# Kernel optimization log

Measured on AMD Instinct MI355X. Metric: run time of the kernel, lower is better.

The kernel has to match this reference:

```python
import jax, jax.numpy as jnp
import numpy as np

N_NODES = 100000
N_EDGES = 1600000
N_GRAPHS = 512
N_REL = 4
N_TYPES = 13
EMB = 128
HID = 128
BN_EPS = 1e-5
L2_EPS = 1e-12


def setup_inputs() -> dict:
    key = jax.random.key(0)
    ks = jax.random.split(key, 16)
    node_type = jax.random.randint(ks[0], (N_NODES,), 0, N_TYPES)
    x = jax.nn.one_hot(node_type, N_TYPES, dtype=jnp.float32)  # [N,13] one-hot
    edge_index = jax.random.randint(ks[1], (2, N_EDGES), 0, N_NODES)
    edge_type = jax.random.randint(ks[2], (N_EDGES,), 0, N_REL)
    batch = jnp.sort(jax.random.randint(ks[3], (N_NODES,), 0, N_GRAPHS))
    s = 0.05
    return {
        "x": x,
        "edge_index": edge_index,
        "edge_type": edge_type,
        "batch": batch,
        "emb": jax.random.normal(ks[4], (N_TYPES, EMB), jnp.float32) * s,
        "Wrel": jax.random.normal(ks[5], (2, N_REL, HID, HID), jnp.float32) * s,  # layer0 in=EMB==HID
        "Wroot": jax.random.normal(ks[6], (2, HID, HID), jnp.float32) * s,
        "conv_bias": jnp.zeros((2, HID), jnp.float32),
        "bn_gamma": jnp.ones((2, HID), jnp.float32),
        "bn_beta": jnp.zeros((2, HID), jnp.float32),
        "prelu_a": jnp.full((2,), 0.25, jnp.float32),
        "fc1_w": jax.random.normal(ks[7], (HID, 256), jnp.float32) * s,
        "fc1_b": jnp.zeros((256,), jnp.float32),
        "fc2_w": jax.random.normal(ks[8], (256, 128), jnp.float32) * s,
        "fc2_b": jnp.zeros((128,), jnp.float32),
        "out_w": jax.random.normal(ks[9], (128, 1), jnp.float32) * s,
        "out_b": jnp.zeros((1,), jnp.float32),
    }


def _rgcn_conv(h, Wrel, Wroot, bias, src, dst, edge_type):
    # PyG RGCNConv: out = h @ Wroot + bias + sum_r mean_{edges of rel r}(h_src @ W_r)
    n = h.shape[0]
    out = h @ Wroot + bias
    for r in range(N_REL):
        m = (edge_type == r).astype(h.dtype)  # [E]
        hr = h @ Wrel[r]                       # [N, dout]
        msg = hr[src] * m[:, None]             # gather + mask  [E, dout]
        num = jax.ops.segment_sum(msg, dst, num_segments=n)
        cnt = jax.ops.segment_sum(m, dst, num_segments=n)
        out = out + num / jnp.maximum(cnt, 1.0)[:, None]
    return out


def _batchnorm(h, gamma, beta):
    mu = jnp.mean(h, axis=0)
    var = jnp.mean((h - mu) ** 2, axis=0)  # biased var (training-mode BN)
    return (h - mu) * jax.lax.rsqrt(var + BN_EPS) * gamma + beta


def reference(x, edge_index, edge_type, batch, emb, Wrel, Wroot, conv_bias,
              bn_gamma, bn_beta, prelu_a, fc1_w, fc1_b, fc2_w, fc2_b, out_w, out_b):
    src, dst = edge_index[0], edge_index[1]
    idx = jnp.argmax(x, axis=1)         # torch.nonzero(one_hot)[1]
    h = emb[idx]                        # [N, EMB]
    for l in range(2):
        h = _rgcn_conv(h, Wrel[l], Wroot[l], conv_bias[l], src, dst, edge_type)
        h = _batchnorm(h, bn_gamma[l], bn_beta[l])
        h = jnp.where(h >= 0, h, prelu_a[l] * h)  # PReLU
        nrm = jnp.sqrt(jnp.sum(h * h, axis=1, keepdims=True))
        h = h / jnp.maximum(nrm, L2_EPS)          # F.normalize(p=2, dim=1)
    # global mean pool over graphs
    pooled = jax.ops.segment_sum(h, batch, num_segments=N_GRAPHS)
    cnt = jax.ops.segment_sum(jnp.ones((h.shape[0],), h.dtype), batch, num_segments=N_GRAPHS)
    g = pooled / jnp.maximum(cnt, 1.0)[:, None]   # [G, HID]
    g = jax.nn.relu(g @ fc1_w + fc1_b)
    g = jax.nn.relu(g @ fc2_w + fc2_b)
    return g @ out_w + out_b                      # [G, 1]
```

## Files before the change

### kernel.cpp

```cpp
#include <hip/hip_runtime.h>
#include <hip/hip_bf16.h>

#define NN 100000
#define NE 1600000
#define NG 512
#define CH3 65536
#define CHW 16384
#define NCH 2
#define BPC 128
#define ES 12500


typedef __attribute__((ext_vector_type(8))) short short8;
typedef __attribute__((ext_vector_type(4))) float float4v;


__device__ inline int lower_bound_dev(const int* __restrict__ a, int n, int v) {
    int lo = 0, hi = n;
    while (lo < hi) { int mid = (lo + hi) >> 1; if (a[mid] < v) lo = mid + 1; else hi = mid; }
    return lo;
}

__device__ inline unsigned short f2bf(float x) {
    unsigned u = __float_as_uint(x);
    unsigned r = (u + 0x7fffu + ((u >> 16) & 1u)) >> 16;
    return (unsigned short)r;
}


__global__ void node_type_kernel(const float* __restrict__ x, int* __restrict__ idx, int n) {
    int i = blockIdx.x * blockDim.x + threadIdx.x;
    if (i >= n) return;
    const float* row = x + (size_t)i * 13;
    int b = 0;
    #pragma unroll
    for (int t = 0; t < 13; ++t) if (row[t] > 0.5f) { b = t; }
    idx[i] = b;
}


__global__ void build_weights(const float* __restrict__ emb, const float* __restrict__ Wroot,
                              const float* __restrict__ Wrel,
                              unsigned short* __restrict__ Bf, unsigned short* __restrict__ B0f,
                              float* __restrict__ bnSums, float* __restrict__ bnSums1,
                              float* __restrict__ g0) {
    if (blockIdx.x < 8) bnSums[blockIdx.x * 256 + threadIdx.x] = 0.f;
    else if (blockIdx.x < 16) bnSums1[(blockIdx.x - 8) * 256 + threadIdx.x] = 0.f;
    int i = blockIdx.x * 256 + threadIdx.x;
    if (i < 81920) {
        int j = i & 7;
        int lane = (i >> 3) & 63;
        int t = (i >> 9) & 7;
        int ks = (i >> 12) & 3;
        int kc = i >> 14;
        int n = t * 16 + (lane & 15);
        int kcol = j * 16 + ks * 4 + (lane >> 4);
        float w;
        if (kc == 0) w = Wroot[16384 + (size_t)kcol * 128 + n];
        else {
            int r = kc - 1;
            w = Wrel[(((size_t)(4 + r) * 128) + kcol) * 128 + n];
        }
        Bf[i] = f2bf(w);
    } else if (i < 94208) {
        int i0 = i - 81920;
        int j = i0 & 7;
        int lane = (i0 >> 3) & 63;
        int t = (i0 >> 9) & 7;
        int ks = i0 >> 12;
        int n = t * 16 + (lane & 15);
        int p = ks * 32 + (lane >> 4) * 8 + j;
        float val = 0.f;
        if (p < 32) {
            if (p < 13) {
                const float* er = emb + (size_t)p * 128;
                const float* wc = Wroot + n;
                float acc = 0.f;
                for (int k = 0; k < 128; ++k) acc += er[k] * wc[(size_t)k * 128];
                val = acc;
            }
        } else {
            int r = (p - 32) >> 4, tt = (p - 32) & 15;
            if (tt < 13) {
                const float* er = emb + (size_t)tt * 128;
                const float* wc = Wrel + ((size_t)r * 128) * 128 + n;
                float acc = 0.f;
                for (int k = 0; k < 128; ++k) acc += er[k] * wc[(size_t)k * 128];
                val = acc;
            }
        }
        B0f[i0] = f2bf(val);
    } else {
        int gz = i - 94208;
        g0[gz] = 0.f;
    }
}


__global__ __launch_bounds__(256) void hist_kernel(const int* __restrict__ dst,
                                                   const int* __restrict__ src,
                                                   const int* __restrict__ et,
                                                   const int* __restrict__ ntype,
                                                   int* __restrict__ srcT,
                                                   unsigned* __restrict__ partials) {
    __shared__ unsigned h[CHW];
    const int b = blockIdx.x, c = blockIdx.y;
    const int lo = c * CH3;
    for (int i = threadIdx.x; i < CHW; i += 256) h[i] = 0;
    __syncthreads();
    const int e0 = b * ES;
    const int e1 = (e0 + ES < NE) ? e0 + ES : NE;
    if (c == 0) {
        for (int e = e0 + threadIdx.x; e < e1; e += 256) {
            int k = dst[e] - lo;
            if (k >= 0 && k < CH3) atomicAdd(&h[k >> 2], 1u << ((k & 3) << 3));
            int s = src[e];
            srcT[e] = s | (ntype[s] << 17) | (et[e] << 21);
        }
    } else {
        for (int e = e0 + threadIdx.x; e < e1; e += 256) {
            int k = dst[e] - lo;
            if (k >= 0 && k < CH3) atomicAdd(&h[k >> 2], 1u << ((k & 3) << 3));
        }
    }
    __syncthreads();
    unsigned* out = partials + ((size_t)(c * BPC + b)) * CHW;
    for (int i = threadIdx.x; i < CHW; i += 256) out[i] = h[i];
}

__global__ void hist_reduce(unsigned* __restrict__ partials, int* __restrict__ counts) {
    const int c = blockIdx.y;
    const int i = blockIdx.x * 256 + threadIdx.x;
    size_t base = (size_t)c * BPC * CHW + i;
    unsigned r0 = 0, r1 = 0, r2 = 0, r3 = 0;
    #pragma unroll 4
    for (int b = 0; b < BPC; ++b) {
        unsigned t = partials[base + (size_t)b * CHW];
        partials[base + (size_t)b * CHW] = r0 | (r1 << 8) | (r2 << 16) | (r3 << 24);
        r0 += t & 0xffu; r1 += (t >> 8) & 0xffu; r2 += (t >> 16) & 0xffu; r3 += t >> 24;
    }
    int k0 = c * CH3 + 4 * i;
    if (k0 < NN)     counts[k0]     = (int)r0;
    if (k0 + 1 < NN) counts[k0 + 1] = (int)r1;
    if (k0 + 2 < NN) counts[k0 + 2] = (int)r2;
    if (k0 + 3 < NN) counts[k0 + 3] = (int)r3;
}

__global__ __launch_bounds__(256) void scan1(const int* __restrict__ counts, int* __restrict__ offs,
                                             int* __restrict__ bsums, int n) {
    __shared__ int wsum[4];
    const int base = blockIdx.x * 1024 + threadIdx.x * 4;
    int v[4]; int loc = 0;
    #pragma unroll
    for (int j = 0; j < 4; ++j) { int idx = base + j; v[j] = (idx < n) ? counts[idx] : 0; loc += v[j]; }
    const int lane = threadIdx.x & 63, wid = threadIdx.x >> 6;
    int sc = loc;
    #pragma unroll
    for (int o = 1; o < 64; o <<= 1) { int t = __shfl_up(sc, o, 64); if (lane >= o) sc += t; }
    if (lane == 63) wsum[wid] = sc;
    __syncthreads();
    int wbase = 0;
    for (int w = 0; w < wid; ++w) wbase += wsum[w];
    int run = wbase + sc - loc;
    #pragma unroll
    for (int j = 0; j < 4; ++j) { int idx = base + j; if (idx < n) offs[idx] = run; run += v[j]; }
    if (threadIdx.x == 255) bsums[blockIdx.x] = wbase + sc;
}

__global__ void scan2(int* __restrict__ bsums, int* __restrict__ offs, int nb, int n) {
    const int lane = threadIdx.x;
    int carry = 0;
    for (int base = 0; base < nb; base += 64) {
        int idx = base + lane;
        int v = (idx < nb) ? bsums[idx] : 0;
        int sc = v;
        #pragma unroll
        for (int o = 1; o < 64; o <<= 1) { int t = __shfl_up(sc, o, 64); if (lane >= o) sc += t; }
        if (idx < nb) bsums[idx] = carry + sc - v;
        int tot = __shfl(sc, 63, 64);
        carry += tot;
    }
    if (lane == 0) offs[n] = carry;
}

__global__ __launch_bounds__(256) void scan3(int* __restrict__ offs, const int* __restrict__ bsums, int n) {
    const int s = bsums[blockIdx.x];
    const int base = blockIdx.x * 1024 + threadIdx.x * 4;
    #pragma unroll
    for (int j = 0; j < 4; ++j) { int idx = base + j; if (idx < n) offs[idx] += s; }
}

__global__ __launch_bounds__(256) void place_kernel(const int* __restrict__ dst,
                                                    const int* __restrict__ srcT,
                                                    const int* __restrict__ offs,
                                                    const unsigned* __restrict__ partials,
                                                    int* __restrict__ sortedSrc) {
    __shared__ unsigned cur[CHW];
    const int b = blockIdx.x, c = blockIdx.y;
    const int lo = c * CH3;
    const unsigned* pb = partials + ((size_t)(c * BPC + b)) * CHW;
    for (int i = threadIdx.x; i < CHW; i += 256) cur[i] = pb[i];
    __syncthreads();
    const int e0 = b * ES;
    const int e1 = (e0 + ES < NE) ? e0 + ES : NE;
    for (int e = e0 + threadIdx.x; e < e1; e += 256) {
        int key = dst[e];
        int k = key - lo;
        if (k >= 0 && k < CH3) {
            int sh = (k & 3) << 3;
            unsigned old = atomicAdd(&cur[k >> 2], 1u << sh);
            int my = (int)((old >> sh) & 0xffu);
            int pos = offs[key] + my;
            sortedSrc[pos] = srcT[e];
        }
    }
}


__global__ __launch_bounds__(256) void gemm0_fused(const int* __restrict__ sortedSrc,
                                                   const int* __restrict__ offs,
                                                   const int* __restrict__ ntype,
                                                   const unsigned short* __restrict__ B0f,
                                                   const float* __restrict__ bias,
                                                   unsigned short* __restrict__ Cb,
                                                   float* __restrict__ bnSums, int M) {
    __shared__ unsigned short A0L[12 * 128 * 8];
    __shared__ unsigned cnt[128][13];
    __shared__ float sred[2][4][128];
    const int tid = threadIdx.x;

    if (tid < 128) {
        const int n = blockIdx.x * 128 + tid;
        const int tile = tid >> 4, l16 = tid & 15;
        if (n < M) {
            #pragma unroll
            for (int t = 0; t < 13; ++t) cnt[tid][t] = 0;
            const int o0 = offs[n], o1 = offs[n + 1];
            unsigned relc = 0;
            for (int i = o0; i < o1; ++i) {
                int v = sortedSrc[i];
                int ty = (v >> 17) & 15, r = v >> 21;
                cnt[tid][ty] += 1u << (r << 3);
                relc += 1u << (r << 3);
            }
            float inv[4];
            #pragma unroll
            for (int r = 0; r < 4; ++r) {
                unsigned c = (relc >> (r << 3)) & 0xffu;
                inv[r] = 1.0f / (float)(c > 0 ? c : 1);
            }
            const int myty = ntype[n];
            #pragma unroll
            for (int ks = 0; ks < 3; ++ks) {
                #pragma unroll
                for (int quad = 0; quad < 4; ++quad) {
                    unsigned short vals[8];
                    #pragma unroll
                    for (int j = 0; j < 8; ++j) {
                        int p = ks * 32 + quad * 8 + j;
                        float v;
                        if (p < 32) v = (p == myty) ? 1.0f : 0.0f;
                        else {
                            int r = (p - 32) >> 4, tt = (p - 32) & 15;
                            v = (tt < 13) ? (float)((cnt[tid][tt] >> (r << 3)) & 0xffu) * inv[r] : 0.0f;
                        }
                        vals[j] = f2bf(v);
                    }
                    const int C = ks * 4 + quad;
                    *(uint4*)(A0L + (C * 128 + tile * 16 + l16) * 8) = *(uint4*)vals;
                }
            }
        } else {
            uint4 z; z.x = 0; z.y = 0; z.z = 0; z.w = 0;
            #pragma unroll
            for (int C = 0; C < 12; ++C)
                *(uint4*)(A0L + (C * 128 + tile * 16 + l16) * 8) = z;
        }
    }
    __syncthreads();

    const int wv = tid >> 6, lane = tid & 63;
    const int l16 = lane & 15, quad = lane >> 4;
    const int rowbase = blockIdx.x * 128 + wv * 32;
    const int tileL0 = wv * 2, tileL1 = wv * 2 + 1;

    float4v acc[2][8];
    #pragma unroll
    for (int t = 0; t < 8; ++t) {
        float bv = bias[t * 16 + l16];
        float4v av = {bv, bv, bv, bv};
        acc[0][t] = av; acc[1][t] = av;
    }

    const unsigned short* bl = B0f + lane * 8;
    #pragma unroll
    for (int ks = 0; ks < 3; ++ks) {
        const int C = ks * 4 + quad;
        short8 af0 = *(const short8*)(A0L + (C * 128 + tileL0 * 16 + l16) * 8);
        short8 af1 = *(const short8*)(A0L + (C * 128 + tileL1 * 16 + l16) * 8);
        const unsigned short* bp = bl + ((ks * 8) << 9);
        #pragma unroll
        for (int t = 0; t < 8; ++t) {
            short8 bf = *(const short8*)(bp + (t << 9));
            acc[0][t] = __builtin_amdgcn_mfma_f32_16x16x32_bf16(af0, bf, acc[0][t], 0, 0, 0);
            acc[1][t] = __builtin_amdgcn_mfma_f32_16x16x32_bf16(af1, bf, acc[1][t], 0, 0, 0);
        }
    }

    #pragma unroll
    for (int h = 0; h < 2; ++h) {
        #pragma unroll
        for (int rg = 0; rg < 4; ++rg) {
            int rr = rowbase + h * 16 + quad * 4 + rg;
            if (rr < M) {
                unsigned short v[8];
                #pragma unroll
                for (int t = 0; t < 8; ++t) v[t] = f2bf(acc[h][t][rg]);
                *(uint4*)(Cb + (size_t)rr * 128 + l16 * 8) = *(uint4*)v;
            }
        }
    }
    float s[8], q[8];
    #pragma unroll
    for (int t = 0; t < 8; ++t) {
        s[t] = 0.f; q[t] = 0.f;
        #pragma unroll
        for (int h = 0; h < 2; ++h) {
            #pragma unroll
            for (int rg = 0; rg < 4; ++rg) {
                int rr = rowbase + h * 16 + quad * 4 + rg;
                if (rr < M) { float v = acc[h][t][rg]; s[t] += v; q[t] += v * v; }
            }
        }
    }
    #pragma unroll
    for (int t = 0; t < 8; ++t) {
        s[t] += __shfl_down(s[t], 32, 64); q[t] += __shfl_down(q[t], 32, 64);
        s[t] += __shfl_down(s[t], 16, 64); q[t] += __shfl_down(q[t], 16, 64);
    }
    if (lane < 16) {
        #pragma unroll
        for (int t = 0; t < 8; ++t) {
            sred[0][wv][t * 16 + l16] = s[t];
            sred[1][wv][t * 16 + l16] = q[t];
        }
    }
    __syncthreads();
    if (tid < 128) {
        float S = sred[0][0][tid] + sred[0][1][tid] + sred[0][2][tid] + sred[0][3][tid];
        float Q = sred[1][0][tid] + sred[1][1][tid] + sred[1][2][tid] + sred[1][3][tid];
        float* bnS = bnSums + ((blockIdx.x & 7) << 8);
        unsafeAtomicAdd(bnS + tid, S);
        unsafeAtomicAdd(bnS + 128 + tid, Q);
    }
}


__global__ __launch_bounds__(256) void gather_gemm1(const unsigned short* __restrict__ hbf,
                                                    const int* __restrict__ sortedSrc,
                                                    const int* __restrict__ offs,
                                                    const unsigned short* __restrict__ Bf,
                                                    const float* __restrict__ bias,
                                                    unsigned short* __restrict__ Cb,
                                                    float* __restrict__ bnSums) {
    __shared__ unsigned short rootL[2048];
    __shared__ unsigned short aggL[8192];
    const int tid = threadIdx.x;
    const int tile = blockIdx.x;
    {
        const int l16g = tid >> 4;
        const int cidx = tid & 15;
        const int c8 = cidx << 3;
        const int n = tile * 16 + l16g;
        const int pu = cidx * 16 + (l16g ^ cidx);
        uint4 ru = *(const uint4*)(hbf + (size_t)n * 128 + c8);
        *(uint4*)(rootL + pu * 8) = ru;

        const unsigned short* hb = hbf + c8;
        const int o0 = offs[n], o1 = offs[n + 1];

        float a0[8], a1[8], a2[8], a3[8];
        #pragma unroll
        for (int j = 0; j < 8; ++j) { a0[j] = 0.f; a1[j] = 0.f; a2[j] = 0.f; a3[j] = 0.f; }
        float c0 = 0.f, c1 = 0.f, c2 = 0.f, c3 = 0.f;

        auto body = [&](int v, uint4 u) {
            int r = v >> 21;
            float f[8];
            f[0] = __uint_as_float(u.x << 16); f[1] = __uint_as_float(u.x & 0xffff0000u);
            f[2] = __uint_as_float(u.y << 16); f[3] = __uint_as_float(u.y & 0xffff0000u);
            f[4] = __uint_as_float(u.z << 16); f[5] = __uint_as_float(u.z & 0xffff0000u);
            f[6] = __uint_as_float(u.w << 16); f[7] = __uint_as_float(u.w & 0xffff0000u);
            float m0 = (r == 0) ? 1.f : 0.f, m1 = (r == 1) ? 1.f : 0.f;
            float m2 = (r == 2) ? 1.f : 0.f, m3 = (r == 3) ? 1.f : 0.f;
            c0 += m0; c1 += m1; c2 += m2; c3 += m3;
            #pragma unroll
            for (int j = 0; j < 8; ++j) {
                a0[j] = fmaf(m0, f[j], a0[j]);
                a1[j] = fmaf(m1, f[j], a1[j]);
                a2[j] = fmaf(m2, f[j], a2[j]);
                a3[j] = fmaf(m3, f[j], a3[j]);
            }
        };

        int i = o0;
        for (; i + 4 <= o1; i += 4) {
            int v0 = sortedSrc[i], v1 = sortedSrc[i + 1];
            int v2 = sortedSrc[i + 2], v3 = sortedSrc[i + 3];
            uint4 u0 = *(const uint4*)(hb + (size_t)(v0 & 0x1ffff) * 128);
            uint4 u1 = *(const uint4*)(hb + (size_t)(v1 & 0x1ffff) * 128);
            uint4 u2 = *(const uint4*)(hb + (size_t)(v2 & 0x1ffff) * 128);
            uint4 u3 = *(const uint4*)(hb + (size_t)(v3 & 0x1ffff) * 128);
            body(v0, u0); body(v1, u1); body(v2, u2); body(v3, u3);
        }
        if (i + 2 <= o1) {
            int v0 = sortedSrc[i], v1 = sortedSrc[i + 1];
            uint4 u0 = *(const uint4*)(hb + (size_t)(v0 & 0x1ffff) * 128);
            uint4 u1 = *(const uint4*)(hb + (size_t)(v1 & 0x1ffff) * 128);
            body(v0, u0); body(v1, u1);
            i += 2;
        }
        if (i < o1) {
            int v0 = sortedSrc[i];
            uint4 u0 = *(const uint4*)(hb + (size_t)(v0 & 0x1ffff) * 128);
            body(v0, u0);
        }

        const float i0 = 1.f / fmaxf(c0, 1.f), i1 = 1.f / fmaxf(c1, 1.f);
        const float i2 = 1.f / fmaxf(c2, 1.f), i3 = 1.f / fmaxf(c3, 1.f);
        unsigned short* bp = aggL + pu * 8;
        auto pack = [&](float* a, float inv, unsigned short* dp) {
            unsigned short v[8];
            #pragma unroll
            for (int j = 0; j < 8; ++j) v[j] = f2bf(a[j] * inv);
            *(uint4*)dp = *(uint4*)v;
        };
        pack(a0, i0, bp);
        pack(a1, i1, bp + 2048);
        pack(a2, i2, bp + 4096);
        pack(a3, i3, bp + 6144);
    }
    __syncthreads();

    const int wv = tid >> 6, lane = tid & 63;
    const int l16 = lane & 15, quad = lane >> 4;
    const int t0 = wv << 1;
    float4v acc0, acc1;
    {
        float b0v = bias[t0 * 16 + l16];
        float b1v = bias[(t0 + 1) * 16 + l16];
        float4v a0v = {b0v, b0v, b0v, b0v};
        float4v a1v = {b1v, b1v, b1v, b1v};
        acc0 = a0v; acc1 = a1v;
    }
    const unsigned short* bl = Bf + lane * 8;
    #pragma unroll
    for (int kc = 0; kc < 5; ++kc) {
        const unsigned short* Abase = (kc == 0) ? rootL : (aggL + (kc - 1) * 2048);
        #pragma unroll
        for (int ks = 0; ks < 4; ++ks) {
            const int C = ks * 4 + quad;
            const int p = C * 16 + (l16 ^ C);
            short8 af = *(const short8*)(Abase + p * 8);
            const unsigned short* bp = bl + (((kc * 4 + ks) * 8 + t0) << 9);
            short8 b0 = *(const short8*)(bp);
            short8 b1 = *(const short8*)(bp + 512);
            acc0 = __builtin_amdgcn_mfma_f32_16x16x32_bf16(af, b0, acc0, 0, 0, 0);
            acc1 = __builtin_amdgcn_mfma_f32_16x16x32_bf16(af, b1, acc1, 0, 0, 0);
        }
    }
    const int rowbase = tile * 16;
    #pragma unroll
    for (int rg = 0; rg < 4; ++rg) {
        int rr = rowbase + quad * 4 + rg;
        unsigned pk = (unsigned)f2bf(acc0[rg]) | ((unsigned)f2bf(acc1[rg]) << 16);
        *(unsigned*)(Cb + (size_t)rr * 128 + l16 * 8 + t0) = pk;
    }
    float s0 = 0.f, q0 = 0.f, s1 = 0.f, q1 = 0.f;
    #pragma unroll
    for (int rg = 0; rg < 4; ++rg) {
        float v0 = acc0[rg], v1 = acc1[rg];
        s0 += v0; q0 += v0 * v0; s1 += v1; q1 += v1 * v1;
    }
    s0 += __shfl_down(s0, 32, 64); q0 += __shfl_down(q0, 32, 64);
    s1 += __shfl_down(s1, 32, 64); q1 += __shfl_down(q1, 32, 64);
    s0 += __shfl_down(s0, 16, 64); q0 += __shfl_down(q0, 16, 64);
    s1 += __shfl_down(s1, 16, 64); q1 += __shfl_down(q1, 16, 64);
    if (lane < 16) {
        float* bnS = bnSums + ((tile & 7) << 8);
        unsafeAtomicAdd(bnS + t0 * 16 + l16, s0);
        unsafeAtomicAdd(bnS + 128 + t0 * 16 + l16, q0);
        unsafeAtomicAdd(bnS + (t0 + 1) * 16 + l16, s1);
        unsafeAtomicAdd(bnS + 128 + (t0 + 1) * 16 + l16, q1);
    }
}


__global__ __launch_bounds__(256) void bn_apply_kernel(const unsigned short* __restrict__ Cb,
                                unsigned short* __restrict__ hbf,
                                const float* __restrict__ bnSums,
                                const float* __restrict__ gamma, const float* __restrict__ beta,
                                const float* __restrict__ prelu_a, int layer) {
    __shared__ float finS[256];
    const int tid = threadIdx.x;
    if (tid < 128) {
        float s = 0.f, q = 0.f;
        #pragma unroll
        for (int j = 0; j < 8; ++j) { s += bnSums[j * 256 + tid]; q += bnSums[j * 256 + 128 + tid]; }
        const float invn = 1.0f / (float)NN;
        float mu = s * invn;
        float var = q * invn - mu * mu; if (var < 0.f) var = 0.f;
        finS[tid] = mu;
        finS[128 + tid] = rsqrtf(var + 1e-5f);
    }
    __syncthreads();
    const int row = blockIdx.x * 16 + (tid >> 4);
    const int li = tid & 15;
    const int p8 = li << 3;
    const float a = prelu_a[layer];
    uint4 u = *(const uint4*)(Cb + (size_t)row * 128 + p8);
    float v[8];
    v[0] = __uint_as_float(u.x << 16); v[1] = __uint_as_float(u.x & 0xffff0000u);
    v[2] = __uint_as_float(u.y << 16); v[3] = __uint_as_float(u.y & 0xffff0000u);
    v[4] = __uint_as_float(u.z << 16); v[5] = __uint_as_float(u.z & 0xffff0000u);
    v[6] = __uint_as_float(u.w << 16); v[7] = __uint_as_float(u.w & 0xffff0000u);
    float t[8]; float ss = 0.f;
    #pragma unroll
    for (int j = 0; j < 8; ++j) {
        int cc = j * 16 + li;
        float tv = (v[j] - finS[cc]) * finS[128 + cc] * gamma[cc] + beta[cc];
        tv = (tv >= 0.f) ? tv : a * tv;
        t[j] = tv; ss += tv * tv;
    }
    ss += __shfl_xor(ss, 1, 64);
    ss += __shfl_xor(ss, 2, 64);
    ss += __shfl_xor(ss, 4, 64);
    ss += __shfl_xor(ss, 8, 64);
    const float scale = 1.0f / fmaxf(sqrtf(ss), 1e-12f);
    unsigned short o[8];
    #pragma unroll
    for (int j = 0; j < 8; ++j) o[j] = f2bf(t[j] * scale);
    *(uint4*)(hbf + (size_t)row * 128 + p8) = *(uint4*)o;
}


__global__ __launch_bounds__(256) void bn_apply_pool(const unsigned short* __restrict__ Cb,
                                const float* __restrict__ bnSums,
                                const float* __restrict__ gamma, const float* __restrict__ beta,
                                const float* __restrict__ prelu_a,
                                const int* __restrict__ batch,
                                float* __restrict__ g0) {
    __shared__ float P[16][128];
    __shared__ int gids[16];
    __shared__ float finS[256];
    const int tid = threadIdx.x;
    if (tid < 128) {
        float s = 0.f, q = 0.f;
        #pragma unroll
        for (int j = 0; j < 8; ++j) { s += bnSums[j * 256 + tid]; q += bnSums[j * 256 + 128 + tid]; }
        const float invn = 1.0f / (float)NN;
        float mu = s * invn;
        float var = q * invn - mu * mu; if (var < 0.f) var = 0.f;
        finS[tid] = mu;
        finS[128 + tid] = rsqrtf(var + 1e-5f);
    }
    const int r16 = tid >> 4;
    const int li = tid & 15;
    const int row = blockIdx.x * 16 + r16;
    const int p8 = li << 3;
    if (li == 0) gids[r16] = batch[row];
    __syncthreads();
    const float a = prelu_a[1];
    uint4 u = *(const uint4*)(Cb + (size_t)row * 128 + p8);
    float v[8];
    v[0] = __uint_as_float(u.x << 16); v[1] = __uint_as_float(u.x & 0xffff0000u);
    v[2] = __uint_as_float(u.y << 16); v[3] = __uint_as_float(u.y & 0xffff0000u);
    v[4] = __uint_as_float(u.z << 16); v[5] = __uint_as_float(u.z & 0xffff0000u);
    v[6] = __uint_as_float(u.w << 16); v[7] = __uint_as_float(u.w & 0xffff0000u);
    float t[8]; float ss = 0.f;
    #pragma unroll
    for (int j = 0; j < 8; ++j) {
        int cc = j * 16 + li;
        float tv = (v[j] - finS[cc]) * finS[128 + cc] * gamma[cc] + beta[cc];
        tv = (tv >= 0.f) ? tv : a * tv;
        t[j] = tv; ss += tv * tv;
    }
    ss += __shfl_xor(ss, 1, 64);
    ss += __shfl_xor(ss, 2, 64);
    ss += __shfl_xor(ss, 4, 64);
    ss += __shfl_xor(ss, 8, 64);
    const float scale = 1.0f / fmaxf(sqrtf(ss), 1e-12f);
    #pragma unroll
    for (int j = 0; j < 8; ++j) P[r16][p8 + j] = t[j] * scale;
    __syncthreads();
    if (tid < 128) {
        int cur = gids[0];
        float run = 0.f;
        #pragma unroll
        for (int rr = 0; rr < 16; ++rr) {
            int g = gids[rr];
            if (g != cur) {
                unsafeAtomicAdd(&g0[(size_t)cur * 128 + tid], run);
                run = 0.f; cur = g;
            }
            run += P[rr][tid];
        }
        unsafeAtomicAdd(&g0[(size_t)cur * 128 + tid], run);
    }
}


__global__ void fc1_kernel(const float* __restrict__ g, const float* __restrict__ w,
                           const float* __restrict__ b, const int* __restrict__ batch,
                           float* __restrict__ o) {
    __shared__ int se[2];
    const int row = blockIdx.x;
    const int j = threadIdx.x;
    if (j < 2) se[j] = lower_bound_dev(batch, NN, row + j);
    __syncthreads();
    const int c = se[1] - se[0];
    const float invc = 1.0f / (float)(c > 0 ? c : 1);
    float acc = 0.f;
    #pragma unroll 8
    for (int k = 0; k < 128; ++k) {
        int lk = (k & 7) * 16 + (k >> 3);
        acc += g[row * 128 + k] * w[lk * 256 + j];
    }
    o[row * 256 + j] = fmaxf(acc * invc + b[j], 0.f);
}

__global__ void fc2_kernel(const float* __restrict__ g, const float* __restrict__ w,
                           const float* __restrict__ b, float* __restrict__ o) {
    const int row = blockIdx.x;
    const int j = threadIdx.x;
    float acc = b[j];
    #pragma unroll 8
    for (int k = 0; k < 256; ++k) acc += g[row * 256 + k] * w[k * 128 + j];
    o[row * 128 + j] = fmaxf(acc, 0.f);
}

__global__ void fco_kernel(const float* __restrict__ g, const float* __restrict__ w,
                           const float* __restrict__ b, float* __restrict__ o) {
    const int row = blockIdx.x * blockDim.x + threadIdx.x;
    if (row >= NG) return;
    float acc = b[0];
    #pragma unroll 8
    for (int k = 0; k < 128; ++k) acc += g[row * 128 + k] * w[k];
    o[row] = acc;
}


extern "C" void kernel_launch(void* const* d_in, const int* in_sizes, int n_in,
                              void* d_out, int out_size, void* d_ws, size_t ws_size,
                              hipStream_t stream) {
    const float* x      = (const float*)d_in[0];
    const int*   eidx   = (const int*)d_in[1];
    const int*   etype  = (const int*)d_in[2];
    const int*   batch  = (const int*)d_in[3];
    const float* emb    = (const float*)d_in[4];
    const float* Wrel   = (const float*)d_in[5];
    const float* Wroot  = (const float*)d_in[6];
    const float* cbias  = (const float*)d_in[7];
    const float* gamma  = (const float*)d_in[8];
    const float* beta   = (const float*)d_in[9];
    const float* prelua = (const float*)d_in[10];
    const float* fc1w   = (const float*)d_in[11];
    const float* fc1b   = (const float*)d_in[12];
    const float* fc2w   = (const float*)d_in[13];
    const float* fc2b   = (const float*)d_in[14];
    const float* outw   = (const float*)d_in[15];
    const float* outb   = (const float*)d_in[16];
    float* out = (float*)d_out;

    const int* src = eidx;
    const int* dst = eidx + NE;

    char* p = (char*)d_ws;
    auto alloc = [&](size_t bytes) { char* r = p; p += (bytes + 255) & ~(size_t)255; return r; };
    unsigned short* hbf   = (unsigned short*)alloc((size_t)NN * 128 * 2);
    unsigned short* Cb    = (unsigned short*)alloc((size_t)NN * 128 * 2);
    unsigned* partials = (unsigned*)alloc((size_t)NCH * BPC * CHW * 4);
    int*   sortedSrc = (int*)alloc((size_t)NE * 4);
    int*   srcT      = (int*)alloc((size_t)NE * 4);
    int*   offs      = (int*)alloc((size_t)(NN + 1) * 4);
    int*   bsums     = (int*)alloc(1024);
    int*   ntype     = (int*)alloc((size_t)NN * 4);
    unsigned short* Bf1 = (unsigned short*)alloc((size_t)81920 * 2);
    unsigned short* B0f = (unsigned short*)alloc((size_t)12288 * 2);
    float* bnSums  = (float*)alloc(2048 * 4);
    float* bnSums1 = (float*)alloc(2048 * 4);
    float* g0      = (float*)alloc((size_t)NG * 128 * 4);
    float* g1      = (float*)alloc((size_t)NG * 256 * 4);
    float* g2      = (float*)alloc((size_t)NG * 128 * 4);

    const int NBLK = (NN + 1023) / 1024;

    node_type_kernel<<<(NN + 255) / 256, 256, 0, stream>>>(x, ntype, NN);
    build_weights<<<624, 256, 0, stream>>>(emb, Wroot, Wrel, Bf1, B0f, bnSums, bnSums1, g0);

    hist_kernel<<<dim3(BPC, NCH), 256, 0, stream>>>(dst, src, etype, ntype, srcT, partials);
    hist_reduce<<<dim3(CHW / 256, NCH), 256, 0, stream>>>(partials, offs);
    scan1<<<NBLK, 256, 0, stream>>>(offs, offs, bsums, NN);
    scan2<<<1, 64, 0, stream>>>(bsums, offs, NBLK, NN);
    scan3<<<NBLK, 256, 0, stream>>>(offs, bsums, NN);
    place_kernel<<<dim3(BPC, NCH), 256, 0, stream>>>(dst, srcT, offs, partials, sortedSrc);

    gemm0_fused<<<(NN + 127) / 128, 256, 0, stream>>>(sortedSrc, offs, ntype, B0f,
                                                      cbias, Cb, bnSums, NN);
    bn_apply_kernel<<<NN / 16, 256, 0, stream>>>(Cb, hbf, bnSums, gamma, beta, prelua, 0);

    gather_gemm1<<<NN / 16, 256, 0, stream>>>(hbf, sortedSrc, offs, Bf1, cbias + 128, Cb, bnSums1);
    bn_apply_pool<<<NN / 16, 256, 0, stream>>>(Cb, bnSums1, gamma + 128, beta + 128,
                                               prelua, batch, g0);

    fc1_kernel<<<NG, 256, 0, stream>>>(g0, fc1w, fc1b, batch, g1);
    fc2_kernel<<<NG, 128, 0, stream>>>(g1, fc2w, fc2b, g2);
    fco_kernel<<<2, 256, 0, stream>>>(g2, outw, outb, out);
}
```

Baseline: 359.3 us.

## Precompute per-node type/relation counts in histogram pass; fuse scans and fc2/out

Layer 0 needs, for each destination node, counts of incoming edges per source node type and relation. These counts are now accumulated with global atomics inside the histogram kernel (zeroed in node_type_kernel), so gemm0 reads a compact count table instead of walking the sorted CSR. The change also merges the two-stage scan carry propagation into one kernel where each block sums the preceding block totals, and fuses fc2 with the final output projection. This removes a serial per-node loop over edges and two kernel launches, in exchange for 1.6M extra global atomics and a 5MB count buffer.

Result: slower. 400.2 us (+11.4%).

```diff
diff --git a/kernel.cpp b/kernel.cpp
--- a/kernel.cpp
+++ b/kernel.cpp
@@ -28,7 +28,8 @@
 }
 
 
-__global__ void node_type_kernel(const float* __restrict__ x, int* __restrict__ idx, int n) {
+__global__ void node_type_kernel(const float* __restrict__ x, int* __restrict__ idx,
+                                 unsigned* __restrict__ cntG, int n) {
     int i = blockIdx.x * blockDim.x + threadIdx.x;
     if (i >= n) return;
     const float* row = x + (size_t)i * 13;
@@ -36,6 +37,9 @@
     #pragma unroll
     for (int t = 0; t < 13; ++t) if (row[t] > 0.5f) { b = t; }
     idx[i] = b;
+    unsigned* c = cntG + (size_t)i * 13;
+    #pragma unroll
+    for (int t = 0; t < 13; ++t) c[t] = 0u;
 }
 
 
@@ -102,6 +106,7 @@
                                                    const int* __restrict__ et,
                                                    const int* __restrict__ ntype,
                                                    int* __restrict__ srcT,
+                                                   unsigned* __restrict__ cntG,
                                                    unsigned* __restrict__ partials) {
     __shared__ unsigned h[CHW];
     const int b = blockIdx.x, c = blockIdx.y;
@@ -112,10 +117,14 @@
     const int e1 = (e0 + ES < NE) ? e0 + ES : NE;
     if (c == 0) {
         for (int e = e0 + threadIdx.x; e < e1; e += 256) {
-            int k = dst[e] - lo;
+            int d = dst[e];
+            int k = d - lo;
             if (k >= 0 && k < CH3) atomicAdd(&h[k >> 2], 1u << ((k & 3) << 3));
             int s = src[e];
-            srcT[e] = s | (ntype[s] << 17) | (et[e] << 21);
+            int ty = ntype[s];
+            int r = et[e];
+            srcT[e] = s | (ty << 17) | (r << 21);
+            atomicAdd(&cntG[(size_t)d * 13 + ty], 1u << (r << 3));
         }
     } else {
         for (int e = e0 + threadIdx.x; e < e1; e += 256) {
@@ -167,27 +176,23 @@
     if (threadIdx.x == 255) bsums[blockIdx.x] = wbase + sc;
 }
 
-__global__ void scan2(int* __restrict__ bsums, int* __restrict__ offs, int nb, int n) {
-    const int lane = threadIdx.x;
-    int carry = 0;
-    for (int base = 0; base < nb; base += 64) {
-        int idx = base + lane;
-        int v = (idx < nb) ? bsums[idx] : 0;
-        int sc = v;
-        #pragma unroll
-        for (int o = 1; o < 64; o <<= 1) { int t = __shfl_up(sc, o, 64); if (lane >= o) sc += t; }
-        if (idx < nb) bsums[idx] = carry + sc - v;
-        int tot = __shfl(sc, 63, 64);
-        carry += tot;
-    }
-    if (lane == 0) offs[n] = carry;
-}
-
-__global__ __launch_bounds__(256) void scan3(int* __restrict__ offs, const int* __restrict__ bsums, int n) {
-    const int s = bsums[blockIdx.x];
-    const int base = blockIdx.x * 1024 + threadIdx.x * 4;
+__global__ __launch_bounds__(256) void scan23(int* __restrict__ offs, const int* __restrict__ bsums,
+                                              int nb, int n) {
+    __shared__ int part[256];
+    const int tid = threadIdx.x;
+    int v = (tid < nb && tid < blockIdx.x) ? bsums[tid] : 0;
+    part[tid] = v;
+    __syncthreads();
+    #pragma unroll
+    for (int o = 128; o > 0; o >>= 1) {
+        if (tid < o) part[tid] += part[tid + o];
+        __syncthreads();
+    }
+    const int s = part[0];
+    const int base = blockIdx.x * 1024 + tid * 4;
     #pragma unroll
     for (int j = 0; j < 4; ++j) { int idx = base + j; if (idx < n) offs[idx] += s; }
+    if (blockIdx.x == (unsigned)(nb - 1) && tid == 0) offs[n] = s + bsums[nb - 1];
 }
 
 __global__ __launch_bounds__(256) void place_kernel(const int* __restrict__ dst,
@@ -217,32 +222,30 @@
 }
 
 
-__global__ __launch_bounds__(256) void gemm0_fused(const int* __restrict__ sortedSrc,
-                                                   const int* __restrict__ offs,
+__global__ __launch_bounds__(256) void gemm0_fused(const unsigned* __restrict__ cntG,
                                                    const int* __restrict__ ntype,
                                                    const unsigned short* __restrict__ B0f,
                                                    const float* __restrict__ bias,
                                                    unsigned short* __restrict__ Cb,
                                                    float* __restrict__ bnSums, int M) {
     __shared__ unsigned short A0L[12 * 128 * 8];
-    __shared__ unsigned cnt[128][13];
+    __shared__ unsigned cls[1664];
     __shared__ float sred[2][4][128];
     const int tid = threadIdx.x;
+
+    {
+        const size_t cbase = (size_t)blockIdx.x * 1664;
+        for (int i = tid; i < 1664; i += 256) cls[i] = cntG[cbase + i];
+    }
+    __syncthreads();
 
     if (tid < 128) {
         const int n = blockIdx.x * 128 + tid;
         const int tile = tid >> 4, l16 = tid & 15;
         if (n < M) {
+            unsigned cw[13]; unsigned relc = 0;
             #pragma unroll
-            for (int t = 0; t < 13; ++t) cnt[tid][t] = 0;
-            const int o0 = offs[n], o1 = offs[n + 1];
-            unsigned relc = 0;
-            for (int i = o0; i < o1; ++i) {
-                int v = sortedSrc[i];
-                int ty = (v >> 17) & 15, r = v >> 21;
-                cnt[tid][ty] += 1u << (r << 3);
-                relc += 1u << (r << 3);
-            }
+            for (int t = 0; t < 13; ++t) { cw[t] = cls[tid * 13 + t]; relc += cw[t]; }
             float inv[4];
             #pragma unroll
             for (int r = 0; r < 4; ++r) {
@@ -262,7 +265,7 @@
                         if (p < 32) v = (p == myty) ? 1.0f : 0.0f;
                         else {
                             int r = (p - 32) >> 4, tt = (p - 32) & 15;
-                            v = (tt < 13) ? (float)((cnt[tid][tt] >> (r << 3)) & 0xffu) * inv[r] : 0.0f;
+                            v = (tt < 13) ? (float)((cw[tt] >> (r << 3)) & 0xffu) * inv[r] : 0.0f;
                         }
                         vals[j] = f2bf(v);
                     }
@@ -629,24 +632,25 @@
     o[row * 256 + j] = fmaxf(acc * invc + b[j], 0.f);
 }
 
-__global__ void fc2_kernel(const float* __restrict__ g, const float* __restrict__ w,
-                           const float* __restrict__ b, float* __restrict__ o) {
+__global__ __launch_bounds__(128) void fc2o_kernel(const float* __restrict__ g, const float* __restrict__ w,
+                            const float* __restrict__ b, const float* __restrict__ outw,
+                            const float* __restrict__ outb, float* __restrict__ out) {
+    __shared__ float wsum[2];
     const int row = blockIdx.x;
     const int j = threadIdx.x;
     float acc = b[j];
     #pragma unroll 8
     for (int k = 0; k < 256; ++k) acc += g[row * 256 + k] * w[k * 128 + j];
-    o[row * 128 + j] = fmaxf(acc, 0.f);
-}
-
-__global__ void fco_kernel(const float* __restrict__ g, const float* __restrict__ w,
-                           const float* __restrict__ b, float* __restrict__ o) {
-    const int row = blockIdx.x * blockDim.x + threadIdx.x;
-    if (row >= NG) return;
-    float acc = b[0];
-    #pragma unroll 8
-    for (int k = 0; k < 128; ++k) acc += g[row * 128 + k] * w[k];
-    o[row] = acc;
+    float c = fmaxf(acc, 0.f) * outw[j];
+    c += __shfl_down(c, 32, 64);
+    c += __shfl_down(c, 16, 64);
+    c += __shfl_down(c, 8, 64);
+    c += __shfl_down(c, 4, 64);
+    c += __shfl_down(c, 2, 64);
+    c += __shfl_down(c, 1, 64);
+    if ((j & 63) == 0) wsum[j >> 6] = c;
+    __syncthreads();
+    if (j == 0) out[row] = wsum[0] + wsum[1] + outb[0];
 }
 
 
@@ -682,6 +686,7 @@
     unsigned* partials = (unsigned*)alloc((size_t)NCH * BPC * CHW * 4);
     int*   sortedSrc = (int*)alloc((size_t)NE * 4);
     int*   srcT      = (int*)alloc((size_t)NE * 4);
+    unsigned* cntG   = (unsigned*)alloc((size_t)782 * 1664 * 4);
     int*   offs      = (int*)alloc((size_t)(NN + 1) * 4);
     int*   bsums     = (int*)alloc(1024);
     int*   ntype     = (int*)alloc((size_t)NN * 4);
@@ -691,22 +696,19 @@
     float* bnSums1 = (float*)alloc(2048 * 4);
     float* g0      = (float*)alloc((size_t)NG * 128 * 4);
     float* g1      = (float*)alloc((size_t)NG * 256 * 4);
-    float* g2      = (float*)alloc((size_t)NG * 128 * 4);
 
     const int NBLK = (NN + 1023) / 1024;
 
-    node_type_kernel<<<(NN + 255) / 256, 256, 0, stream>>>(x, ntype, NN);
+    node_type_kernel<<<(NN + 255) / 256, 256, 0, stream>>>(x, ntype, cntG, NN);
     build_weights<<<624, 256, 0, stream>>>(emb, Wroot, Wrel, Bf1, B0f, bnSums, bnSums1, g0);
 
-    hist_kernel<<<dim3(BPC, NCH), 256, 0, stream>>>(dst, src, etype, ntype, srcT, partials);
+    hist_kernel<<<dim3(BPC, NCH), 256, 0, stream>>>(dst, src, etype, ntype, srcT, cntG, partials);
     hist_reduce<<<dim3(CHW / 256, NCH), 256, 0, stream>>>(partials, offs);
     scan1<<<NBLK, 256, 0, stream>>>(offs, offs, bsums, NN);
-    scan2<<<1, 64, 0, stream>>>(bsums, offs, NBLK, NN);
-    scan3<<<NBLK, 256, 0, stream>>>(offs, bsums, NN);
+    scan23<<<NBLK, 256, 0, stream>>>(offs, bsums, NBLK, NN);
     place_kernel<<<dim3(BPC, NCH), 256, 0, stream>>>(dst, srcT, offs, partials, sortedSrc);
 
-    gemm0_fused<<<(NN + 127) / 128, 256, 0, stream>>>(sortedSrc, offs, ntype, B0f,
-                                                      cbias, Cb, bnSums, NN);
+    gemm0_fused<<<(NN + 127) / 128, 256, 0, stream>>>(cntG, ntype, B0f, cbias, Cb, bnSums, NN);
     bn_apply_kernel<<<NN / 16, 256, 0, stream>>>(Cb, hbf, bnSums, gamma, beta, prelua, 0);
 
     gather_gemm1<<<NN / 16, 256, 0, stream>>>(hbf, sortedSrc, offs, Bf1, cbias + 128, Cb, bnSums1);
@@ -714,6 +716,5 @@
                                                prelua, batch, g0);
 
     fc1_kernel<<<NG, 256, 0, stream>>>(g0, fc1w, fc1b, batch, g1);
-    fc2_kernel<<<NG, 128, 0, stream>>>(g1, fc2w, fc2b, g2);
-    fco_kernel<<<2, 256, 0, stream>>>(g2, outw, outb, out);
-}
+    fc2o_kernel<<<NG, 128, 0, stream>>>(g1, fc2w, fc2b, outw, outb, out);
+}
```
